# Kernel optimization log

Hardware: AMD Instinct MI355X
Metric: run time of the kernel (lower is better)

## Reference

```python
import jax, jax.numpy as jnp
import numpy as np

H, B, C, R, L, A, NEAR = 4, 8, 64, 64, 2048, 8, 2
EPS = 1e-5

def setup_inputs() -> dict:
    key = jax.random.key(0)
    ks = jax.random.split(key, 16)
    d = {}
    d['inputs'] = jax.random.normal(ks[0], (H, B, C, L), jnp.float32)
    d['hidden'] = jax.random.normal(ks[1], (B, R, L), jnp.float32)
    # per-head spatial attention 1x1 convs (no bias)
    d['key_w'] = jax.random.normal(ks[2], (H, R, C), jnp.float32) * 0.05
    d['value_w'] = jax.random.normal(ks[3], (H, C, C), jnp.float32) * 0.05
    # channel attention (1x1 convs with bias)
    HC = H * C
    d['ca_w1'] = jax.random.normal(ks[4], (A, HC + R), jnp.float32) * 0.05
    d['ca_b1'] = jnp.zeros((A,), jnp.float32)
    d['ca_w2'] = jax.random.normal(ks[5], (HC, A), jnp.float32) * 0.05
    d['ca_b2'] = jnp.zeros((HC,), jnp.float32)
    # projection: conv3(no bias) -> BN -> relu -> conv3(no bias) -> BN -> relu
    d['pw1'] = jax.random.normal(ks[6], (R, HC, 3), jnp.float32) * 0.02
    d['bn1_g'] = jnp.ones((R,), jnp.float32)
    d['bn1_b'] = jnp.zeros((R,), jnp.float32)
    d['bn1_m'] = jnp.zeros((R,), jnp.float32)
    d['bn1_v'] = jnp.ones((R,), jnp.float32)
    d['pw2'] = jax.random.normal(ks[7], (R, R, 3), jnp.float32) * 0.02
    d['bn2_g'] = jnp.ones((R,), jnp.float32)
    d['bn2_b'] = jnp.zeros((R,), jnp.float32)
    d['bn2_m'] = jnp.zeros((R,), jnp.float32)
    d['bn2_v'] = jnp.ones((R,), jnp.float32)
    return d

def _bn(x, g, b, m, v):
    # eval-mode BatchNorm1d over channel dim of [B,C,L]
    inv = g / jnp.sqrt(v + EPS)
    return x * inv[None, :, None] + (b - m * inv)[None, :, None]

def _conv3(x, w):
    # [B,Cin,L] x [Cout,Cin,3] -> [B,Cout,L], padding=1
    return jax.lax.conv_general_dilated(x, w, (1,), 'SAME',
                                        dimension_numbers=('NCH', 'OIH', 'NCH'))

def reference(inputs, hidden, key_w, value_w, ca_w1, ca_b1, ca_w2, ca_b2,
              pw1, bn1_g, bn1_b, bn1_m, bn1_v, pw2, bn2_g, bn2_b, bn2_m, bn2_v):
    scale = 1.0 / jnp.sqrt(jnp.float32(R))
    # spatial attention, vectorized over heads
    k = jnp.einsum('hrc,hbcl->hbrl', key_w, inputs)      # keys
    v = jnp.einsum('hoc,hbcl->hbol', value_w, inputs)    # values
    q = hidden * scale                                   # [B,R,L]
    attn = jnp.einsum('brl,hbrm->hblm', q, k)            # [H,B,L,L]
    idx = jnp.arange(L)
    band = (jnp.abs(idx[:, None] - idx[None, :]) <= NEAR).astype(attn.dtype)
    attn = jax.nn.softmax(attn * band, axis=-1)          # multiplicative mask then softmax (faithful)
    val = jnp.einsum('hbcl,hblm->hbcm', v, attn)
    enc = inputs + val                                   # dropout in eval = identity
    x = jnp.transpose(enc, (1, 0, 2, 3)).reshape(B, H * C, L)  # concat heads on channel
    # channel attention gating
    cat = jnp.concatenate([x, hidden], axis=1)           # [B,HC+R,L]
    a = jax.nn.relu(jnp.einsum('oc,bcl->bol', ca_w1, cat) + ca_b1[None, :, None])
    gate = jax.nn.sigmoid(jnp.einsum('oa,bal->bol', ca_w2, a) + ca_b2[None, :, None])
    x = x * gate
    # projection
    y = jax.nn.relu(_bn(_conv3(x, pw1), bn1_g, bn1_b, bn1_m, bn1_v))
    y = jax.nn.relu(_bn(_conv3(y, pw2), bn2_g, bn2_b, bn2_m, bn2_v))
    return y
```

## Files before the change

### kernel.cpp

```cpp
#include <hip/hip_runtime.h>
#include <hip/hip_bf16.h>
#include <math.h>

#define HH 4
#define BB 8
#define CC 64
#define RR 64
#define LL 2048
#define AA 8
#define HC 256
#define EPS 1e-5f
#define CHP 266

typedef unsigned short ushort_t;
typedef __attribute__((ext_vector_type(8))) short short8;
typedef __attribute__((ext_vector_type(4))) float f32x4;

static __device__ __forceinline__ ushort_t f2bf(float x) {
    unsigned u = __float_as_uint(x);
    unsigned r = (u + 0x7FFF + ((u >> 16) & 1)) >> 16;
    return (ushort_t)r;
}
static __device__ __forceinline__ float bf2f(ushort_t h) {
    return __uint_as_float(((unsigned)h) << 16);
}
static __device__ __forceinline__ void pack8(const float* p, short8& hi, short8& lo) {
    float4 x0 = *(const float4*)p;
    float4 x1 = *(const float4*)(p + 4);
    float xs[8] = {x0.x, x0.y, x0.z, x0.w, x1.x, x1.y, x1.z, x1.w};
#pragma unroll
    for (int e = 0; e < 8; ++e) {
        ushort_t h = f2bf(xs[e]);
        hi[e] = (short)h;
        lo[e] = (short)f2bf(xs[e] - bf2f(h));
    }
}

__global__ __launch_bounds__(256, 4) void kABC(const float* __restrict__ inp,
                                               const float* __restrict__ kw,
                                               const float* __restrict__ vw,
                                               const float* __restrict__ hidden,
                                               float* __restrict__ XC,
                                               float* __restrict__ Spart,
                                               const float* __restrict__ pw1,
                                               const float* __restrict__ g1,
                                               const float* __restrict__ m1,
                                               const float* __restrict__ v1,
                                               const float* __restrict__ bb1,
                                               const float* __restrict__ pw2,
                                               const float* __restrict__ g2,
                                               const float* __restrict__ m2,
                                               const float* __restrict__ v2,
                                               const float* __restrict__ bb2,
                                               const float* __restrict__ w1ca,
                                               ushort_t* __restrict__ wEb,
                                               ushort_t* __restrict__ wFb,
                                               float* __restrict__ biasE,
                                               float* __restrict__ biasF,
                                               float* __restrict__ w1T) {
    if (blockIdx.x == 32) {
        int tid = blockIdx.y * 256 + threadIdx.x;
        const int stride = 64 * 256;
        for (int idx = tid; idx < 4 * 24 * 64 * 8; idx += stride) {
            int j = idx & 7, lane = (idx >> 3) & 63, t2 = idx >> 9;
            int ks = t2 % 24, rg = t2 / 24;
            int r = rg * 16 + (lane & 15);
            int k = ks * 32 + (lane >> 4) * 8 + j;
            int tap = k >> 8, ch = k & 255;
            float inv = g1[r] * rsqrtf(v1[r] + EPS);
            wEb[idx] = f2bf(pw1[(r * 256 + ch) * 3 + tap] * inv);
        }
        for (int idx = tid; idx < 4 * 6 * 64 * 8; idx += stride) {
            int j = idx & 7, lane = (idx >> 3) & 63, t2 = idx >> 9;
            int ks = t2 % 6, rg = t2 / 6;
            int r = rg * 16 + (lane & 15);
            int k = ks * 32 + (lane >> 4) * 8 + j;
            int tap = k >> 6, c = k & 63;
            float inv = g2[r] * rsqrtf(v2[r] + EPS);
            wFb[idx] = f2bf(pw2[(r * 64 + c) * 3 + tap] * inv);
        }
        for (int idx = tid; idx < 320 * 8; idx += stride)
            w1T[idx] = w1ca[(idx & 7) * 320 + (idx >> 3)];
        if (tid < 64) {
            float inv1 = g1[tid] * rsqrtf(v1[tid] + EPS);
            biasE[tid] = bb1[tid] - m1[tid] * inv1;
            float inv2 = g2[tid] * rsqrtf(v2[tid] + EPS);
            biasF[tid] = bb2[tid] - m2[tid] * inv2;
        }
        return;
    }
    int hb = blockIdx.x;
    int h = hb >> 3;
    int b = hb & 7;
    int l0 = blockIdx.y * 32;
    __shared__ __align__(16) char shbuf[2 * 48 * 72 * 2];
    ushort_t (*xsT)[48][72] = (ushort_t (*)[48][72])shbuf;
    float (*k_s)[44] = (float (*)[44])shbuf;
    __shared__ float partial[4][36][5];
    __shared__ float dw_s[36][5];
    __shared__ float u_s[36];
    __shared__ float red_s[64];
    int t = threadIdx.x;
    int lane = t & 63, wv = t >> 6;
    int a = lane & 15, kg = lane >> 4;
    short8 ah[2][2], al[2][2];
    {
        const float* kwh = kw + h * 4096;
        const float* vwh = vw + h * 4096;
#pragma unroll
        for (int rtl = 0; rtl < 2; ++rtl) {
            int rt = wv * 2 + rtl;
            int row = rt * 16 + a;
            const float* base = (rt < 4) ? (kwh + row * 64) : (vwh + (row - 64) * 64);
#pragma unroll
            for (int ks = 0; ks < 2; ++ks)
                pack8(base + ks * 32 + kg * 8, ah[rtl][ks], al[rtl][ks]);
        }
    }
    {
        float xv[12];
#pragma unroll
        for (int it = 0; it < 12; ++it) {
            int idx = t + it * 256;
            int ch = idx / 48, j = idx % 48;
            int l = l0 - 4 + j;
            xv[it] = (j < 40 && l >= 0 && l < LL)
                   ? inp[(size_t)(hb * 64 + ch) * LL + l] : 0.f;
        }
#pragma unroll
        for (int it = 0; it < 12; ++it) {
            int idx = t + it * 256;
            int ch = idx / 48, j = idx % 48;
            ushort_t hi = f2bf(xv[it]);
            xsT[0][j][ch] = hi;
            xsT[1][j][ch] = f2bf(xv[it] - bf2f(hi));
        }
    }
    __syncthreads();
    f32x4 acc[2][3] = {};
#pragma unroll
    for (int ks = 0; ks < 2; ++ks) {
#pragma unroll
        for (int ct = 0; ct < 3; ++ct) {
            short8 bhf = *(const short8*)&xsT[0][ct * 16 + a][ks * 32 + kg * 8];
            short8 blf = *(const short8*)&xsT[1][ct * 16 + a][ks * 32 + kg * 8];
#pragma unroll
            for (int rtl = 0; rtl < 2; ++rtl) {
                acc[rtl][ct] = __builtin_amdgcn_mfma_f32_16x16x32_bf16(ah[rtl][ks], bhf, acc[rtl][ct], 0, 0, 0);
                acc[rtl][ct] = __builtin_amdgcn_mfma_f32_16x16x32_bf16(ah[rtl][ks], blf, acc[rtl][ct], 0, 0, 0);
                acc[rtl][ct] = __builtin_amdgcn_mfma_f32_16x16x32_bf16(al[rtl][ks], bhf, acc[rtl][ct], 0, 0, 0);
            }
        }
    }
    __syncthreads();
#pragma unroll
    for (int rtl = 0; rtl < 2; ++rtl) {
        int rt = wv * 2 + rtl;
        if (rt < 4) {
#pragma unroll
            for (int ct = 0; ct < 3; ++ct) {
                int j = ct * 16 + a;
#pragma unroll
                for (int reg = 0; reg < 4; ++reg) {
                    int row = rt * 16 + kg * 4 + reg;
                    if (j < 44) k_s[row][j] = acc[rtl][ct][reg];
                }
            }
        }
    }
    __syncthreads();
    if (lane < 36) {
        float acc5[5] = {};
        int l = l0 - 2 + lane;
        int lc = min(max(l, 0), LL - 1);
        const float* hp = hidden + (size_t)(b * 64 + wv * 16) * LL + lc;
#pragma unroll 4
        for (int i = 0; i < 16; ++i) {
            float hh = hp[(size_t)i * LL];
            int r = wv * 16 + i;
            acc5[0] += hh * k_s[r][lane];
            acc5[1] += hh * k_s[r][lane + 1];
            acc5[2] += hh * k_s[r][lane + 2];
            acc5[3] += hh * k_s[r][lane + 3];
            acc5[4] += hh * k_s[r][lane + 4];
        }
#pragma unroll
        for (int d = 0; d < 5; ++d) partial[wv][lane][d] = acc5[d];
    }
    __syncthreads();
    if (t < 36) {
        int l = l0 - 2 + t;
        if (l < 0 || l >= LL) {
            u_s[t] = 0.f;
#pragma unroll
            for (int d = 0; d < 5; ++d) dw_s[t][d] = 0.f;
        } else {
            float raw[5];
            float mx = 0.f;
            int nv = 0;
#pragma unroll
            for (int d = 0; d < 5; ++d) {
                float s = partial[0][t][d] + partial[1][t][d]
                        + partial[2][t][d] + partial[3][t][d];
                int m = l + d - 2;
                bool valid = (m >= 0 && m < LL);
                raw[d] = valid ? s * 0.125f : -1e30f;
                if (valid) { nv++; mx = fmaxf(mx, raw[d]); }
            }
            float e0 = __expf(-mx);
            float Z = (float)(LL - nv) * e0;
            float w[5];
#pragma unroll
            for (int d = 0; d < 5; ++d) {
                float e = (raw[d] > -1e29f) ? __expf(raw[d] - mx) : 0.f;
                w[d] = e;
                Z += e;
            }
            float inv = 1.f / Z;
            float u = e0 * inv;
            u_s[t] = u;
#pragma unroll
            for (int d = 0; d < 5; ++d) dw_s[t][d] = w[d] * inv - u;
        }
    }
    __syncthreads();
    if (wv >= 2) {
#pragma unroll
        for (int rtl = 0; rtl < 2; ++rtl) {
            int vr0 = (wv * 2 + rtl - 4) * 16 + kg * 4;
#pragma unroll
            for (int ct = 0; ct < 3; ++ct) {
                int j = ct * 16 + a;
#pragma unroll
                for (int reg = 0; reg < 4; ++reg) {
                    if (j >= 2 && j < 38) k_s[vr0 + reg][j] = acc[rtl][ct][reg];
                }
            }
#pragma unroll
            for (int reg = 0; reg < 4; ++reg) {
                float s = 0.f;
#pragma unroll
                for (int ct = 0; ct < 3; ++ct) {
                    int j = ct * 16 + a;
                    if (j >= 4 && j < 36) s += acc[rtl][ct][reg] * u_s[j - 2];
                }
                s += __shfl_xor(s, 1);
                s += __shfl_xor(s, 2);
                s += __shfl_xor(s, 4);
                s += __shfl_xor(s, 8);
                if (a == 0) red_s[vr0 + reg] = s;
            }
        }
    }
    __syncthreads();
    {
        int mm = t & 31;
        int cq = t >> 5;
#pragma unroll
        for (int it = 0; it < 8; ++it) {
            int c = it * 8 + cq;
            float xc = 0.f;
#pragma unroll
            for (int o = -2; o <= 2; ++o)
                xc += k_s[c][mm - o + 4] * dw_s[mm - o + 2][o + 2];
            XC[(size_t)(hb * 64 + c) * LL + l0 + mm] = xc;
        }
    }
    if (t < 64)
        Spart[((size_t)hb * 64 + blockIdx.y) * 64 + t] = red_s[t];
}

__global__ __launch_bounds__(512) void kD(const float* __restrict__ inp,
                                          const float* __restrict__ hidden,
                                          const float* __restrict__ XC,
                                          const float* __restrict__ Spart,
                                          const float* __restrict__ w1T,
                                          const float* __restrict__ b1,
                                          const float* __restrict__ w2,
                                          const float* __restrict__ b2,
                                          float* __restrict__ XG) {
    int b = blockIdx.x;
    int m0 = blockIdx.y * 64;
    __shared__ float S2_s[256];
    __shared__ float partial[8][64][9];
    int t = threadIdx.x;
    int m = t & 63;
    int wv = t >> 6;
    if (t < 256) {
        int hb = (t >> 6) * 8 + b;
        float s = 0.f;
#pragma unroll
        for (int q = 0; q < 64; ++q)
            s += Spart[((size_t)hb * 64 + q) * 64 + (t & 63)];
        S2_s[t] = s;
    }
    __syncthreads();
    float xr[4][8];
    int cb = __builtin_amdgcn_readfirstlane(wv * 8);
#pragma unroll
    for (int h = 0; h < 4; ++h) {
#pragma unroll
        for (int cc = 0; cc < 8; ++cc) {
            int c = cb + cc;
            size_t idx = (size_t)((h * 8 + b) * 64 + c) * LL + m0 + m;
            xr[h][cc] = inp[idx] + XC[idx] + S2_s[h * 64 + c];
        }
    }
    float acc2[8] = {};
#pragma unroll
    for (int h = 0; h < 4; ++h) {
#pragma unroll
        for (int cc = 0; cc < 8; ++cc) {
            const float* wp = w1T + (h * 64 + cb + cc) * 8;
            float xv = xr[h][cc];
#pragma unroll
            for (int o = 0; o < 8; ++o) acc2[o] += wp[o] * xv;
        }
    }
#pragma unroll
    for (int i = 0; i < 8; ++i) {
        const float* wp = w1T + (256 + cb + i) * 8;
        float xv = hidden[(size_t)(b * 64 + cb + i) * LL + m0 + m];
#pragma unroll
        for (int o = 0; o < 8; ++o) acc2[o] += wp[o] * xv;
    }
#pragma unroll
    for (int o = 0; o < 8; ++o) partial[wv][m][o] = acc2[o];
    __syncthreads();
    float a[8];
#pragma unroll
    for (int o = 0; o < 8; ++o) {
        float v = b1[o];
#pragma unroll
        for (int p = 0; p < 8; ++p) v += partial[p][m][o];
        a[o] = fmaxf(v, 0.f);
    }
#pragma unroll
    for (int h = 0; h < 4; ++h) {
#pragma unroll
        for (int cc = 0; cc < 8; ++cc) {
            int ch = h * 64 + cb + cc;
            const float* wp = w2 + ch * 8;
            float g = b2[ch];
#pragma unroll
            for (int o = 0; o < 8; ++o) g += wp[o] * a[o];
            float gate = 1.f / (1.f + __expf(-g));
            XG[(size_t)(b * 256 + ch) * LL + m0 + m] = xr[h][cc] * gate;
        }
    }
}

__global__ __launch_bounds__(256) void kConvM(const float* __restrict__ XG,
                                              const ushort_t* __restrict__ wEb,
                                              const float* __restrict__ biasE,
                                              float* __restrict__ Y1) {
    int b = blockIdx.x;
    int l0 = blockIdx.y * 16;
    __shared__ ushort_t xts[2][18][CHP];
    __shared__ float bias_s[64];
    int t = threadIdx.x;
    if (t < 64) bias_s[t] = biasE[t];
    for (int q = t; q < 18 * 64; q += 256) {
        int row = q % 18;
        int ch0 = (q / 18) * 4;
        int l = l0 - 1 + row;
        bool v = (l >= 0 && l < LL);
        unsigned hp[2], lp[2];
#pragma unroll
        for (int p = 0; p < 2; ++p) {
            unsigned h2 = 0, l2 = 0;
#pragma unroll
            for (int i = 0; i < 2; ++i) {
                int ch = ch0 + p * 2 + i;
                float x = v ? XG[(size_t)(b * 256 + ch) * LL + l] : 0.f;
                ushort_t hi = f2bf(x);
                ushort_t lo = f2bf(x - bf2f(hi));
                h2 |= ((unsigned)hi) << (16 * i);
                l2 |= ((unsigned)lo) << (16 * i);
            }
            hp[p] = h2; lp[p] = l2;
        }
        *(unsigned*)&xts[0][row][ch0] = hp[0];
        *(unsigned*)&xts[0][row][ch0 + 2] = hp[1];
        *(unsigned*)&xts[1][row][ch0] = lp[0];
        *(unsigned*)&xts[1][row][ch0 + 2] = lp[1];
    }
    __syncthreads();
    int lane = t & 63;
    int wid = t >> 6;
    int a = lane & 15;
    int kg = lane >> 4;
    f32x4 acc = {};
    union U8 { unsigned u[4]; short8 s; };
#pragma unroll 4
    for (int ks = 0; ks < 24; ++ks) {
        int tap = ks >> 3;
        int ch0 = ((ks & 7) << 5) + (kg << 3);
        const ushort_t* ap = wEb + ((((size_t)wid * 24 + ks) * 64 + lane) << 3);
        short8 afr = *(const short8*)ap;
        int row = a + tap;
        const ushort_t* xh = &xts[0][row][ch0];
        const ushort_t* xl = &xts[1][row][ch0];
        U8 bh, bl;
#pragma unroll
        for (int qq = 0; qq < 4; ++qq) {
            bh.u[qq] = *(const unsigned*)(xh + 2 * qq);
            bl.u[qq] = *(const unsigned*)(xl + 2 * qq);
        }
        acc = __builtin_amdgcn_mfma_f32_16x16x32_bf16(afr, bh.s, acc, 0, 0, 0);
        acc = __builtin_amdgcn_mfma_f32_16x16x32_bf16(afr, bl.s, acc, 0, 0, 0);
    }
    {
        int m = a;
#pragma unroll
        for (int reg = 0; reg < 4; ++reg) {
            int r = wid * 16 + kg * 4 + reg;
            float y = acc[reg] + bias_s[r];
            Y1[(size_t)(b * 64 + r) * LL + l0 + m] = fmaxf(y, 0.f);
        }
    }
}

__global__ __launch_bounds__(256) void kCM2(const float* __restrict__ Y1,
                                            const ushort_t* __restrict__ wFb,
                                            const float* __restrict__ biasF,
                                            float* __restrict__ out) {
    int b = blockIdx.x;
    int l0 = blockIdx.y * 32;
    __shared__ ushort_t yts[2][34][70];
    __shared__ float bias_s[64];
    int t = threadIdx.x;
    if (t < 64) bias_s[t] = biasF[t];
    for (int q = t; q < 34 * 16; q += 256) {
        int row = q % 34;
        int c0 = (q / 34) * 4;
        int l = l0 - 1 + row;
        bool v = (l >= 0 && l < LL);
        unsigned hp[2], lp[2];
#pragma unroll
        for (int p = 0; p < 2; ++p) {
            unsigned h2 = 0, l2 = 0;
#pragma unroll
            for (int i = 0; i < 2; ++i) {
                int c = c0 + p * 2 + i;
                float x = v ? Y1[(size_t)(b * 64 + c) * LL + l] : 0.f;
                ushort_t hi = f2bf(x);
                ushort_t lo = f2bf(x - bf2f(hi));
                h2 |= ((unsigned)hi) << (16 * i);
                l2 |= ((unsigned)lo) << (16 * i);
            }
            hp[p] = h2; lp[p] = l2;
        }
        *(unsigned*)&yts[0][row][c0] = hp[0];
        *(unsigned*)&yts[0][row][c0 + 2] = hp[1];
        *(unsigned*)&yts[1][row][c0] = lp[0];
        *(unsigned*)&yts[1][row][c0 + 2] = lp[1];
    }
    __syncthreads();
    int lane = t & 63;
    int wid = t >> 6;
    int wm = wid & 1, wn = wid >> 1;
    int a = lane & 15;
    int kg = lane >> 4;
    f32x4 acc[2] = {};
    union U8 { unsigned u[4]; short8 s; };
#pragma unroll
    for (int ks = 0; ks < 6; ++ks) {
        int tap = ks >> 1;
        int c0 = ((ks & 1) << 5) + (kg << 3);
        short8 afr[2];
#pragma unroll
        for (int tr = 0; tr < 2; ++tr) {
            const ushort_t* ap = wFb + ((((size_t)(wm * 2 + tr) * 6 + ks) * 64 + lane) << 3);
            afr[tr] = *(const short8*)ap;
        }
        int s = wn * 16 + a + tap;
        const ushort_t* yh = &yts[0][s][c0];
        const ushort_t* yl = &yts[1][s][c0];
        U8 bh, bl;
#pragma unroll
        for (int qq = 0; qq < 4; ++qq) {
            bh.u[qq] = *(const unsigned*)(yh + 2 * qq);
            bl.u[qq] = *(const unsigned*)(yl + 2 * qq);
        }
#pragma unroll
        for (int tr = 0; tr < 2; ++tr) {
            acc[tr] = __builtin_amdgcn_mfma_f32_16x16x32_bf16(afr[tr], bh.s, acc[tr], 0, 0, 0);
            acc[tr] = __builtin_amdgcn_mfma_f32_16x16x32_bf16(afr[tr], bl.s, acc[tr], 0, 0, 0);
        }
    }
#pragma unroll
    for (int tr = 0; tr < 2; ++tr) {
        int m = wn * 16 + a;
#pragma unroll
        for (int reg = 0; reg < 4; ++reg) {
            int r = wm * 32 + tr * 16 + kg * 4 + reg;
            float y = acc[tr][reg] + bias_s[r];
            out[(size_t)(b * 64 + r) * LL + l0 + m] = fmaxf(y, 0.f);
        }
    }
}

extern "C" void kernel_launch(void* const* d_in, const int* in_sizes, int n_in,
                              void* d_out, int out_size, void* d_ws, size_t ws_size,
                              hipStream_t stream) {
    (void)in_sizes; (void)n_in; (void)out_size; (void)ws_size;
    const float* inp    = (const float*)d_in[0];
    const float* hidden = (const float*)d_in[1];
    const float* key_w  = (const float*)d_in[2];
    const float* value_w= (const float*)d_in[3];
    const float* ca_w1  = (const float*)d_in[4];
    const float* ca_b1  = (const float*)d_in[5];
    const float* ca_w2  = (const float*)d_in[6];
    const float* ca_b2  = (const float*)d_in[7];
    const float* pw1    = (const float*)d_in[8];
    const float* bn1_g  = (const float*)d_in[9];
    const float* bn1_b  = (const float*)d_in[10];
    const float* bn1_m  = (const float*)d_in[11];
    const float* bn1_v  = (const float*)d_in[12];
    const float* pw2    = (const float*)d_in[13];
    const float* bn2_g  = (const float*)d_in[14];
    const float* bn2_b  = (const float*)d_in[15];
    const float* bn2_m  = (const float*)d_in[16];
    const float* bn2_v  = (const float*)d_in[17];

    float* ws = (float*)d_ws;
    const size_t KV = (size_t)HH * BB * CC * LL;
    float* XG = ws;
    float* XC = ws + KV;
    float* Spart = ws + 2 * KV;
    float* w1T   = Spart + 131072;
    float* biasE = w1T + 2560;
    float* biasF = biasE + 64;
    ushort_t* wEb = (ushort_t*)(biasF + 64);
    ushort_t* wFb = (ushort_t*)(biasF + 64 + 24576);
    float* Y1 = XC;

    kABC<<<dim3(33, 64), 256, 0, stream>>>(inp, key_w, value_w, hidden,
                                           XC, Spart,
                                           pw1, bn1_g, bn1_m, bn1_v, bn1_b,
                                           pw2, bn2_g, bn2_m, bn2_v, bn2_b,
                                           ca_w1, wEb, wFb, biasE, biasF, w1T);
    kD<<<dim3(BB, LL / 64), 512, 0, stream>>>(inp, hidden, XC, Spart,
                                              w1T, ca_b1, ca_w2, ca_b2, XG);
    kConvM<<<dim3(BB, 128), 256, 0, stream>>>(XG, wEb, biasE, Y1);
    kCM2<<<dim3(BB, 64), 256, 0, stream>>>(Y1, wFb, biasF, (float*)d_out);
}
```

Measured before the change: 64.82 us.

## Fuse channel-attention gating into first conv kernel and atomically reduce row sums

Merges the channel-attention gating kernel into the first 3-tap projection conv kernel. Each conv tile now recomputes the gate for its 18-column halo from X0 and hidden in shared memory instead of round-tripping the gated XG tensor through global memory. kABC now writes inputs+xc directly and reduces the per-tile sums with atomicAdd into a small buffer, which is cleared by a memset. This removes one launch and a full-size intermediate write and read, at the cost of redundant halo gating work, atomics, and higher shared-memory use per block.

```diff
diff --git a/kernel.cpp b/kernel.cpp
--- a/kernel.cpp
+++ b/kernel.cpp
@@ -40,8 +40,8 @@
                                                const float* __restrict__ kw,
                                                const float* __restrict__ vw,
                                                const float* __restrict__ hidden,
-                                               float* __restrict__ XC,
-                                               float* __restrict__ Spart,
+                                               float* __restrict__ X0,
+                                               float* __restrict__ S,
                                                const float* __restrict__ pw1,
                                                const float* __restrict__ g1,
                                                const float* __restrict__ m1,
@@ -263,127 +263,114 @@
 #pragma unroll
             for (int o = -2; o <= 2; ++o)
                 xc += k_s[c][mm - o + 4] * dw_s[mm - o + 2][o + 2];
-            XC[(size_t)(hb * 64 + c) * LL + l0 + mm] = xc;
-        }
-    }
-    if (t < 64)
-        Spart[((size_t)hb * 64 + blockIdx.y) * 64 + t] = red_s[t];
-}
-
-__global__ __launch_bounds__(512) void kD(const float* __restrict__ inp,
-                                          const float* __restrict__ hidden,
-                                          const float* __restrict__ XC,
-                                          const float* __restrict__ Spart,
-                                          const float* __restrict__ w1T,
-                                          const float* __restrict__ b1,
-                                          const float* __restrict__ w2,
-                                          const float* __restrict__ b2,
-                                          float* __restrict__ XG) {
-    int b = blockIdx.x;
-    int m0 = blockIdx.y * 64;
-    __shared__ float S2_s[256];
-    __shared__ float partial[8][64][9];
-    int t = threadIdx.x;
-    int m = t & 63;
-    int wv = t >> 6;
-    if (t < 256) {
-        int hb = (t >> 6) * 8 + b;
-        float s = 0.f;
-#pragma unroll
-        for (int q = 0; q < 64; ++q)
-            s += Spart[((size_t)hb * 64 + q) * 64 + (t & 63)];
-        S2_s[t] = s;
-    }
-    __syncthreads();
-    float xr[4][8];
-    int cb = __builtin_amdgcn_readfirstlane(wv * 8);
-#pragma unroll
-    for (int h = 0; h < 4; ++h) {
-#pragma unroll
-        for (int cc = 0; cc < 8; ++cc) {
-            int c = cb + cc;
-            size_t idx = (size_t)((h * 8 + b) * 64 + c) * LL + m0 + m;
-            xr[h][cc] = inp[idx] + XC[idx] + S2_s[h * 64 + c];
-        }
-    }
-    float acc2[8] = {};
-#pragma unroll
-    for (int h = 0; h < 4; ++h) {
-#pragma unroll
-        for (int cc = 0; cc < 8; ++cc) {
-            const float* wp = w1T + (h * 64 + cb + cc) * 8;
-            float xv = xr[h][cc];
-#pragma unroll
-            for (int o = 0; o < 8; ++o) acc2[o] += wp[o] * xv;
-        }
-    }
-#pragma unroll
-    for (int i = 0; i < 8; ++i) {
-        const float* wp = w1T + (256 + cb + i) * 8;
-        float xv = hidden[(size_t)(b * 64 + cb + i) * LL + m0 + m];
-#pragma unroll
-        for (int o = 0; o < 8; ++o) acc2[o] += wp[o] * xv;
-    }
-#pragma unroll
-    for (int o = 0; o < 8; ++o) partial[wv][m][o] = acc2[o];
-    __syncthreads();
-    float a[8];
-#pragma unroll
-    for (int o = 0; o < 8; ++o) {
-        float v = b1[o];
-#pragma unroll
-        for (int p = 0; p < 8; ++p) v += partial[p][m][o];
-        a[o] = fmaxf(v, 0.f);
-    }
-#pragma unroll
-    for (int h = 0; h < 4; ++h) {
-#pragma unroll
-        for (int cc = 0; cc < 8; ++cc) {
-            int ch = h * 64 + cb + cc;
-            const float* wp = w2 + ch * 8;
-            float g = b2[ch];
-#pragma unroll
-            for (int o = 0; o < 8; ++o) g += wp[o] * a[o];
-            float gate = 1.f / (1.f + __expf(-g));
-            XG[(size_t)(b * 256 + ch) * LL + m0 + m] = xr[h][cc] * gate;
-        }
-    }
-}
-
-__global__ __launch_bounds__(256) void kConvM(const float* __restrict__ XG,
-                                              const ushort_t* __restrict__ wEb,
-                                              const float* __restrict__ biasE,
-                                              float* __restrict__ Y1) {
+            size_t gi = (size_t)(hb * 64 + c) * LL + l0 + mm;
+            X0[gi] = inp[gi] + xc;
+        }
+    }
+    if (t < 64) atomicAdd(&S[hb * 64 + t], red_s[t]);
+}
+
+__global__ __launch_bounds__(256) void kDC1(const float* __restrict__ X0,
+                                            const float* __restrict__ hidden,
+                                            const float* __restrict__ S,
+                                            const float* __restrict__ w1T,
+                                            const float* __restrict__ b1,
+                                            const float* __restrict__ w2,
+                                            const float* __restrict__ b2,
+                                            const ushort_t* __restrict__ wEb,
+                                            const float* __restrict__ biasE,
+                                            float* __restrict__ Y1) {
     int b = blockIdx.x;
     int l0 = blockIdx.y * 16;
-    __shared__ ushort_t xts[2][18][CHP];
+    __shared__ float x_s[320][19];
+    __shared__ __align__(16) char shb[2 * 18 * CHP * 2];
+    ushort_t (*xts)[18][CHP] = (ushort_t (*)[18][CHP])shb;
+    float (*partial)[32][9] = (float (*)[32][9])shb;
+    __shared__ float S_s[256];
+    __shared__ float a_s[32][9];
     __shared__ float bias_s[64];
     int t = threadIdx.x;
     if (t < 64) bias_s[t] = biasE[t];
-    for (int q = t; q < 18 * 64; q += 256) {
-        int row = q % 18;
-        int ch0 = (q / 18) * 4;
-        int l = l0 - 1 + row;
-        bool v = (l >= 0 && l < LL);
-        unsigned hp[2], lp[2];
-#pragma unroll
-        for (int p = 0; p < 2; ++p) {
-            unsigned h2 = 0, l2 = 0;
-#pragma unroll
-            for (int i = 0; i < 2; ++i) {
-                int ch = ch0 + p * 2 + i;
-                float x = v ? XG[(size_t)(b * 256 + ch) * LL + l] : 0.f;
-                ushort_t hi = f2bf(x);
-                ushort_t lo = f2bf(x - bf2f(hi));
-                h2 |= ((unsigned)hi) << (16 * i);
-                l2 |= ((unsigned)lo) << (16 * i);
-            }
-            hp[p] = h2; lp[p] = l2;
-        }
-        *(unsigned*)&xts[0][row][ch0] = hp[0];
-        *(unsigned*)&xts[0][row][ch0 + 2] = hp[1];
-        *(unsigned*)&xts[1][row][ch0] = lp[0];
-        *(unsigned*)&xts[1][row][ch0 + 2] = lp[1];
+    S_s[t] = S[((t >> 6) * 8 + b) * 64 + (t & 63)];
+    float xv[18];
+#pragma unroll
+    for (int k = 0; k < 18; ++k) {
+        int idx = t + k * 256;
+        int ch = idx / 18, col = idx % 18;
+        int l = l0 - 1 + col;
+        xv[k] = (l >= 0 && l < LL)
+              ? X0[(size_t)((((ch >> 6) * 8 + b) * 64) + (ch & 63)) * LL + l] : 0.f;
+    }
+    float hv[5];
+#pragma unroll
+    for (int k = 0; k < 5; ++k) {
+        int idx = t + k * 256;
+        hv[k] = 0.f;
+        if (idx < 1152) {
+            int r = idx / 18, col = idx % 18;
+            int l = l0 - 1 + col;
+            if (l >= 0 && l < LL) hv[k] = hidden[(size_t)(b * 64 + r) * LL + l];
+        }
+    }
+    __syncthreads();
+#pragma unroll
+    for (int k = 0; k < 18; ++k) {
+        int idx = t + k * 256;
+        int ch = idx / 18, col = idx % 18;
+        int l = l0 - 1 + col;
+        x_s[ch][col] = (l >= 0 && l < LL) ? (xv[k] + S_s[ch]) : 0.f;
+    }
+#pragma unroll
+    for (int k = 0; k < 5; ++k) {
+        int idx = t + k * 256;
+        if (idx < 1152) {
+            int r = idx / 18, col = idx % 18;
+            x_s[256 + r][col] = hv[k];
+        }
+    }
+    __syncthreads();
+    {
+        int col = t & 31;
+        int g = t >> 5;
+        float acc8[8] = {};
+        if (col < 18) {
+            for (int i = 0; i < 40; ++i) {
+                int ch = g * 40 + i;
+                float xval = x_s[ch][col];
+                const float* wp = w1T + ch * 8;
+                float4 wa = *(const float4*)wp;
+                float4 wb = *(const float4*)(wp + 4);
+                acc8[0] += wa.x * xval; acc8[1] += wa.y * xval;
+                acc8[2] += wa.z * xval; acc8[3] += wa.w * xval;
+                acc8[4] += wb.x * xval; acc8[5] += wb.y * xval;
+                acc8[6] += wb.z * xval; acc8[7] += wb.w * xval;
+            }
+        }
+#pragma unroll
+        for (int o = 0; o < 8; ++o) partial[g][col][o] = acc8[o];
+    }
+    __syncthreads();
+    if (t < 144) {
+        int c2 = t / 8, o = t & 7;
+        float v = b1[o];
+#pragma unroll
+        for (int g2 = 0; g2 < 8; ++g2) v += partial[g2][c2][o];
+        a_s[c2][o] = fmaxf(v, 0.f);
+    }
+    __syncthreads();
+#pragma unroll
+    for (int k = 0; k < 18; ++k) {
+        int idx = t + k * 256;
+        int ch = idx / 18, col = idx % 18;
+        const float* wp = w2 + ch * 8;
+        float gg = b2[ch];
+#pragma unroll
+        for (int o = 0; o < 8; ++o) gg += wp[o] * a_s[col][o];
+        float gate = 1.f / (1.f + __expf(-gg));
+        float xg = x_s[ch][col] * gate;
+        ushort_t hi = f2bf(xg);
+        xts[0][col][ch] = hi;
+        xts[1][col][ch] = f2bf(xg - bf2f(hi));
     }
     __syncthreads();
     int lane = t & 63;
@@ -526,23 +513,22 @@
 
     float* ws = (float*)d_ws;
     const size_t KV = (size_t)HH * BB * CC * LL;
-    float* XG = ws;
-    float* XC = ws + KV;
-    float* Spart = ws + 2 * KV;
-    float* w1T   = Spart + 131072;
+    float* Y1 = ws;
+    float* X0 = ws + KV;
+    float* S  = ws + 2 * KV;
+    float* w1T   = S + 2048;
     float* biasE = w1T + 2560;
     float* biasF = biasE + 64;
     ushort_t* wEb = (ushort_t*)(biasF + 64);
     ushort_t* wFb = (ushort_t*)(biasF + 64 + 24576);
-    float* Y1 = XC;
-
+
+    hipMemsetAsync(S, 0, 2048 * sizeof(float), stream);
     kABC<<<dim3(33, 64), 256, 0, stream>>>(inp, key_w, value_w, hidden,
-                                           XC, Spart,
+                                           X0, S,
                                            pw1, bn1_g, bn1_m, bn1_v, bn1_b,
                                            pw2, bn2_g, bn2_m, bn2_v, bn2_b,
                                            ca_w1, wEb, wFb, biasE, biasF, w1T);
-    kD<<<dim3(BB, LL / 64), 512, 0, stream>>>(inp, hidden, XC, Spart,
-                                              w1T, ca_b1, ca_w2, ca_b2, XG);
-    kConvM<<<dim3(BB, 128), 256, 0, stream>>>(XG, wEb, biasE, Y1);
+    kDC1<<<dim3(BB, 128), 256, 0, stream>>>(X0, hidden, S, w1T, ca_b1,
+                                            ca_w2, ca_b2, wEb, biasE, Y1);
     kCM2<<<dim3(BB, 64), 256, 0, stream>>>(Y1, wFb, biasF, (float*)d_out);
 }
```

Result: slower. 71.81 us (+10.8%).

## Fuse residual add into kABC, atomically reduce S, shrink kD blocks

Applied to the files above, without the earlier changes.

kABC now writes X0 = inputs + local correction directly and reduces the per-block partial sums into a small S buffer with atomicAdd instead of writing 64 partials per head-batch. kD therefore reads one array instead of two and skips the 64-way Spart reduction. Its blocks shrink to 256 threads over 32 positions, doubling the grid. The change adds a memset launch and atomic contention on S, and Y1 moves to a separate workspace buffer so the output no longer aliases X0.

```diff
diff --git a/kernel.cpp b/kernel.cpp
--- a/kernel.cpp
+++ b/kernel.cpp
@@ -40,8 +40,8 @@
                                                const float* __restrict__ kw,
                                                const float* __restrict__ vw,
                                                const float* __restrict__ hidden,
-                                               float* __restrict__ XC,
-                                               float* __restrict__ Spart,
+                                               float* __restrict__ X0,
+                                               float* __restrict__ S,
                                                const float* __restrict__ pw1,
                                                const float* __restrict__ g1,
                                                const float* __restrict__ m1,
@@ -263,47 +263,39 @@
 #pragma unroll
             for (int o = -2; o <= 2; ++o)
                 xc += k_s[c][mm - o + 4] * dw_s[mm - o + 2][o + 2];
-            XC[(size_t)(hb * 64 + c) * LL + l0 + mm] = xc;
-        }
-    }
-    if (t < 64)
-        Spart[((size_t)hb * 64 + blockIdx.y) * 64 + t] = red_s[t];
-}
-
-__global__ __launch_bounds__(512) void kD(const float* __restrict__ inp,
+            size_t gi = (size_t)(hb * 64 + c) * LL + l0 + mm;
+            X0[gi] = inp[gi] + xc;
+        }
+    }
+    if (t < 64) atomicAdd(&S[hb * 64 + t], red_s[t]);
+}
+
+__global__ __launch_bounds__(256) void kD(const float* __restrict__ X0,
                                           const float* __restrict__ hidden,
-                                          const float* __restrict__ XC,
-                                          const float* __restrict__ Spart,
+                                          const float* __restrict__ S,
                                           const float* __restrict__ w1T,
                                           const float* __restrict__ b1,
                                           const float* __restrict__ w2,
                                           const float* __restrict__ b2,
                                           float* __restrict__ XG) {
     int b = blockIdx.x;
-    int m0 = blockIdx.y * 64;
-    __shared__ float S2_s[256];
-    __shared__ float partial[8][64][9];
+    int m0 = blockIdx.y * 32;
+    __shared__ float S_s[256];
+    __shared__ float partial[8][32][9];
     int t = threadIdx.x;
-    int m = t & 63;
-    int wv = t >> 6;
-    if (t < 256) {
-        int hb = (t >> 6) * 8 + b;
-        float s = 0.f;
-#pragma unroll
-        for (int q = 0; q < 64; ++q)
-            s += Spart[((size_t)hb * 64 + q) * 64 + (t & 63)];
-        S2_s[t] = s;
-    }
+    int m = t & 31;
+    int g = t >> 5;
+    int cb = g * 8;
+    S_s[t] = S[((t >> 6) * 8 + b) * 64 + (t & 63)];
     __syncthreads();
     float xr[4][8];
-    int cb = __builtin_amdgcn_readfirstlane(wv * 8);
 #pragma unroll
     for (int h = 0; h < 4; ++h) {
 #pragma unroll
         for (int cc = 0; cc < 8; ++cc) {
             int c = cb + cc;
             size_t idx = (size_t)((h * 8 + b) * 64 + c) * LL + m0 + m;
-            xr[h][cc] = inp[idx] + XC[idx] + S2_s[h * 64 + c];
+            xr[h][cc] = X0[idx] + S_s[h * 64 + c];
         }
     }
     float acc2[8] = {};
@@ -325,7 +317,7 @@
         for (int o = 0; o < 8; ++o) acc2[o] += wp[o] * xv;
     }
 #pragma unroll
-    for (int o = 0; o < 8; ++o) partial[wv][m][o] = acc2[o];
+    for (int o = 0; o < 8; ++o) partial[g][m][o] = acc2[o];
     __syncthreads();
     float a[8];
 #pragma unroll
@@ -341,10 +333,10 @@
         for (int cc = 0; cc < 8; ++cc) {
             int ch = h * 64 + cb + cc;
             const float* wp = w2 + ch * 8;
-            float g = b2[ch];
-#pragma unroll
-            for (int o = 0; o < 8; ++o) g += wp[o] * a[o];
-            float gate = 1.f / (1.f + __expf(-g));
+            float gg = b2[ch];
+#pragma unroll
+            for (int o = 0; o < 8; ++o) gg += wp[o] * a[o];
+            float gate = 1.f / (1.f + __expf(-gg));
             XG[(size_t)(b * 256 + ch) * LL + m0 + m] = xr[h][cc] * gate;
         }
     }
@@ -527,22 +519,25 @@
     float* ws = (float*)d_ws;
     const size_t KV = (size_t)HH * BB * CC * LL;
     float* XG = ws;
-    float* XC = ws + KV;
-    float* Spart = ws + 2 * KV;
-    float* w1T   = Spart + 131072;
+    float* X0 = ws + KV;
+    float* Y1 = X0;
+    float* Y1b = ws + 2 * KV;
+    float* S  = ws + 3 * KV;
+    float* w1T   = S + 2048;
     float* biasE = w1T + 2560;
     float* biasF = biasE + 64;
     ushort_t* wEb = (ushort_t*)(biasF + 64);
     ushort_t* wFb = (ushort_t*)(biasF + 64 + 24576);
-    float* Y1 = XC;
-
+    (void)Y1;
+
+    hipMemsetAsync(S, 0, 2048 * sizeof(float), stream);
     kABC<<<dim3(33, 64), 256, 0, stream>>>(inp, key_w, value_w, hidden,
-                                           XC, Spart,
+                                           X0, S,
                                            pw1, bn1_g, bn1_m, bn1_v, bn1_b,
                                            pw2, bn2_g, bn2_m, bn2_v, bn2_b,
                                            ca_w1, wEb, wFb, biasE, biasF, w1T);
-    kD<<<dim3(BB, LL / 64), 512, 0, stream>>>(inp, hidden, XC, Spart,
-                                              w1T, ca_b1, ca_w2, ca_b2, XG);
-    kConvM<<<dim3(BB, 128), 256, 0, stream>>>(XG, wEb, biasE, Y1);
-    kCM2<<<dim3(BB, 64), 256, 0, stream>>>(Y1, wFb, biasF, (float*)d_out);
-}
+    kD<<<dim3(BB, 64), 256, 0, stream>>>(X0, hidden, S, w1T, ca_b1,
+                                         ca_w2, ca_b2, XG);
+    kConvM<<<dim3(BB, 128), 256, 0, stream>>>(XG, wEb, biasE, Y1b);
+    kCM2<<<dim3(BB, 64), 256, 0, stream>>>(Y1b, wFb, biasF, (float*)d_out);
+}
```

Measured after the change: 76.85 us. 1.19x slower.
